# Kernel optimization log

Measured on AMD Instinct MI355X. Metric: run time of the kernel, lower is better.

Reference implementation:

```python
import jax, jax.numpy as jnp
import numpy as np

N_NODES = 100000


def sage_conv(x, edge_index, Wl, bl, Wr):
    # PyG SAGEConv (aggr='mean', root_weight=True):
    #   out_i = lin_l(mean_{j in N(i)} x_j) + lin_r(x_i)
    src, dst = edge_index[0], edge_index[1]
    msgs = x[src]  # [E, C] gather of source-node features
    summed = jax.ops.segment_sum(msgs, dst, num_segments=N_NODES)
    deg = jax.ops.segment_sum(jnp.ones((edge_index.shape[1],), x.dtype), dst,
                              num_segments=N_NODES)
    mean = summed / jnp.maximum(deg, 1.0)[:, None]  # zero rows stay zero
    return mean @ Wl.T + bl + x @ Wr.T


def setup_inputs() -> dict:
    key = jax.random.key(0)
    ks = jax.random.split(key, 12)
    IN, HID, OUT = 128, 128, 64
    E, P = 1600000, 200000
    x = jax.random.normal(ks[0], (N_NODES, IN), jnp.float32)
    edge_index = jax.random.randint(ks[1], (2, E), 0, N_NODES)
    edge_label_index = jax.random.randint(ks[2], (2, P), 0, N_NODES)
    s1 = 1.0 / np.sqrt(IN)
    s2 = 1.0 / np.sqrt(HID)
    s3 = 1.0 / np.sqrt(2 * OUT)
    return {
        "x": x,
        "edge_index": edge_index,
        "edge_label_index": edge_label_index,
        "Wl1": jax.random.uniform(ks[3], (HID, IN), jnp.float32, -s1, s1),
        "bl1": jnp.zeros((HID,), jnp.float32),
        "Wr1": jax.random.uniform(ks[4], (HID, IN), jnp.float32, -s1, s1),
        "Wl2": jax.random.uniform(ks[5], (OUT, HID), jnp.float32, -s2, s2),
        "bl2": jnp.zeros((OUT,), jnp.float32),
        "Wr2": jax.random.uniform(ks[6], (OUT, HID), jnp.float32, -s2, s2),
        "Wdec": jax.random.uniform(ks[7], (1, 2 * OUT), jnp.float32, -s3, s3),
        "bdec": jax.random.uniform(ks[8], (1,), jnp.float32, -s3, s3),
    }


def reference(x, edge_index, edge_label_index, Wl1, bl1, Wr1, Wl2, bl2, Wr2,
              Wdec, bdec):
    # encode: SAGEConv -> relu -> (dropout p=0) -> SAGEConv
    h = jax.nn.relu(sage_conv(x, edge_index, Wl1, bl1, Wr1))
    z = sage_conv(h, edge_index, Wl2, bl2, Wr2)
    # decode: gather endpoint embeddings, concat, linear -> [P]
    feats = jnp.concatenate([z[edge_label_index[0]], z[edge_label_index[1]]],
                            axis=-1)
    return (feats @ Wdec.T + bdec).reshape(-1)
```

## Files before the change

kernel.cpp:

```cpp
#include <hip/hip_runtime.h>

#define NN 100000
#define NBUK ((NN + 255) / 256)
#define BCAP 5120

typedef unsigned short u16;
typedef unsigned int u32;
typedef __attribute__((ext_vector_type(8))) short short8v;
typedef __attribute__((ext_vector_type(4))) float float4v;

__device__ __forceinline__ u32 f2bf_rne(float f) {
    u32 x = __float_as_uint(f);
    return (x + 0x7fffu + ((x >> 16) & 1u)) >> 16;
}
__device__ __forceinline__ float bf2f(u32 u) {
    return __uint_as_float(u << 16);
}
__device__ __forceinline__ uint4 pack8u(const float4& a, const float4& b) {
    uint4 u;
    u.x = f2bf_rne(a.x) | (f2bf_rne(a.y) << 16);
    u.y = f2bf_rne(a.z) | (f2bf_rne(a.w) << 16);
    u.z = f2bf_rne(b.x) | (f2bf_rne(b.y) << 16);
    u.w = f2bf_rne(b.z) | (f2bf_rne(b.w) << 16);
    return u;
}

__global__ void zero_buckets_kernel(int* __restrict__ p) {
    int i = threadIdx.x;
    if (i < NBUK) p[i] = 0;
}

__global__ __launch_bounds__(256) void partition_kernel(const int* __restrict__ edges,
                                                        int* __restrict__ bucketCnt,
                                                        int* __restrict__ bucketed, int E) {
    __shared__ int h[NBUK];
    __shared__ int base[NBUK];
    for (int i = threadIdx.x; i < NBUK; i += 256) h[i] = 0;
    __syncthreads();
    int b0 = blockIdx.x * 4096;
    for (int k = threadIdx.x; k < 4096; k += 256) {
        int e = b0 + k;
        if (e < E) atomicAdd(&h[edges[E + e] >> 8], 1);
    }
    __syncthreads();
    for (int i = threadIdx.x; i < NBUK; i += 256) {
        int c = h[i];
        base[i] = c ? (i * BCAP + atomicAdd(&bucketCnt[i], c)) : 0;
        h[i] = 0;
    }
    __syncthreads();
    for (int k = threadIdx.x; k < 4096; k += 256) {
        int e = b0 + k;
        if (e < E) {
            int d = edges[E + e];
            int b = d >> 8;
            int off = atomicAdd(&h[b], 1);
            bucketed[base[b] + off] = edges[e] | ((d & 255) << 20);
        }
    }
}

__global__ __launch_bounds__(256) void bucket_sort_kernel(const int* __restrict__ bucketed,
                                                          const int* __restrict__ bucketCnt,
                                                          int* __restrict__ rowStart,
                                                          int* __restrict__ cnt,
                                                          int* __restrict__ sortedSrc, int N) {
    __shared__ int h[256];
    __shared__ int pos[256];
    int b = blockIdx.x;
    int tid = threadIdx.x;
    int start = b * BCAP, end = start + bucketCnt[b];
    h[tid] = 0;
    __syncthreads();
    for (int k = start + tid; k < end; k += 256) atomicAdd(&h[bucketed[k] >> 20], 1);
    __syncthreads();
    int v = h[tid];
    pos[tid] = v;
    __syncthreads();
    for (int off = 1; off < 256; off <<= 1) {
        int t = (tid >= off) ? pos[tid - off] : 0;
        __syncthreads();
        pos[tid] += t;
        __syncthreads();
    }
    int excl = start + pos[tid] - v;
    int node = (b << 8) + tid;
    if (node < N) {
        rowStart[node] = excl;
        cnt[node] = v;
    }
    h[tid] = excl;
    __syncthreads();
    for (int k = start + tid; k < end; k += 256) {
        int entry = bucketed[k];
        int p = atomicAdd(&h[entry >> 20], 1);
        sortedSrc[p] = entry & 0xFFFFF;
    }
}

template <bool XF32>
__global__ __launch_bounds__(256, 2) void gemm_mfma_kernel(
    const void* __restrict__ Xv, const float* __restrict__ Wa,
    const float* __restrict__ Wb, int CHALF,
    u16* __restrict__ Ob, int OSTRIDE, int N)
{
    __shared__ u16 As[128 * 128];

    const int tid = threadIdx.x;
    const int w = tid >> 6;
    const int l = tid & 63;
    const int l15 = l & 15;
    const int lhi = l >> 4;
    const int rowBase = blockIdx.x * 128;
    const int cBase = blockIdx.y * 128;
    char* asb = reinterpret_cast<char*>(As);

#pragma unroll
    for (int i = 0; i < 8; ++i) {
        int q = tid + i * 256;
        int r = q >> 4, c = q & 15;
        int gr = rowBase + r;
        uint4 pk = make_uint4(0u, 0u, 0u, 0u);
        if (gr < N) {
            if (XF32) {
                const float* xf = (const float*)Xv + (size_t)gr * 128 + c * 8;
                float4 f0 = *reinterpret_cast<const float4*>(xf);
                float4 f1 = *reinterpret_cast<const float4*>(xf + 4);
                pk = pack8u(f0, f1);
            } else {
                pk = *reinterpret_cast<const uint4*>((const u16*)Xv + (size_t)gr * 128 + c * 8);
            }
        }
        *reinterpret_cast<uint4*>(asb + r * 256 + ((c * 16) ^ ((r & 7) << 4))) = pk;
    }

    short8v bfrag[2][4];
#pragma unroll
    for (int nj = 0; nj < 2; ++nj) {
        int c = cBase + w * 32 + nj * 16 + l15;
        const float* wr = (c < CHALF) ? (Wa + (size_t)c * 128)
                                      : (Wb + (size_t)(c - CHALF) * 128);
#pragma unroll
        for (int kk = 0; kk < 4; ++kk) {
            float4 f0 = *reinterpret_cast<const float4*>(wr + kk * 32 + lhi * 8);
            float4 f1 = *reinterpret_cast<const float4*>(wr + kk * 32 + lhi * 8 + 4);
            uint4 pk = pack8u(f0, f1);
            union { uint4 u; short8v s; } cv; cv.u = pk;
            bfrag[nj][kk] = cv.s;
        }
    }

    __syncthreads();

    float4v acc[8][2];
    const float4v az = {0.f, 0.f, 0.f, 0.f};
#pragma unroll
    for (int mi = 0; mi < 8; ++mi) { acc[mi][0] = az; acc[mi][1] = az; }

#pragma unroll
    for (int kk = 0; kk < 4; ++kk) {
#pragma unroll
        for (int mi = 0; mi < 8; ++mi) {
            int r = mi * 16 + l15;
            short8v a = *reinterpret_cast<const short8v*>(
                asb + r * 256 + ((kk * 64 + lhi * 16) ^ ((r & 7) << 4)));
            acc[mi][0] = __builtin_amdgcn_mfma_f32_16x16x32_bf16(a, bfrag[0][kk], acc[mi][0], 0, 0, 0);
            acc[mi][1] = __builtin_amdgcn_mfma_f32_16x16x32_bf16(a, bfrag[1][kk], acc[mi][1], 0, 0, 0);
        }
    }

#pragma unroll
    for (int mi = 0; mi < 8; ++mi) {
#pragma unroll
        for (int nj = 0; nj < 2; ++nj) {
            int gc = cBase + w * 32 + nj * 16 + l15;
#pragma unroll
            for (int j = 0; j < 4; ++j) {
                int gr = rowBase + mi * 16 + lhi * 4 + j;
                if (gr < N) Ob[(size_t)gr * OSTRIDE + gc] = (u16)f2bf_rne(acc[mi][nj][j]);
            }
        }
    }
}

template <bool RELU>
__global__ __launch_bounds__(256) void agg_combine_kernel(
    const u16* __restrict__ T, int tStride,
    const u16* __restrict__ R,
    const int* __restrict__ sortedSrc, const int* __restrict__ rowStart,
    const int* __restrict__ cnt, const float* __restrict__ bias,
    u16* __restrict__ outB, int oStride, int N)
{
    constexpr int TPN = 8;
    constexpr int NPB = 256 / TPN;
    int n = blockIdx.x * NPB + threadIdx.x / TPN;
    int c = threadIdx.x % TPN;
    if (n >= N) return;
    int start = rowStart[n];
    int m = cnt[n];
    const int* __restrict__ ep = sortedSrc + start;
    const u16* __restrict__ tp = T + c * 8;

    float a0 = 0.f, a1 = 0.f, a2 = 0.f, a3 = 0.f;
    float a4 = 0.f, a5 = 0.f, a6 = 0.f, a7 = 0.f;
    int k = 0;
    for (; k + 8 <= m; k += 8) {
        int s[8];
        uint4 v[8];
#pragma unroll
        for (int u = 0; u < 8; ++u) s[u] = ep[k + u];
#pragma unroll
        for (int u = 0; u < 8; ++u)
            v[u] = *reinterpret_cast<const uint4*>(&tp[(size_t)s[u] * tStride]);
#pragma unroll
        for (int h = 0; h < 2; ++h) {
            const uint4& w0 = v[h * 4 + 0]; const uint4& w1 = v[h * 4 + 1];
            const uint4& w2 = v[h * 4 + 2]; const uint4& w3 = v[h * 4 + 3];
            a0 += bf2f(w0.x & 0xffffu) + bf2f(w1.x & 0xffffu) + bf2f(w2.x & 0xffffu) + bf2f(w3.x & 0xffffu);
            a1 += bf2f(w0.x >> 16) + bf2f(w1.x >> 16) + bf2f(w2.x >> 16) + bf2f(w3.x >> 16);
            a2 += bf2f(w0.y & 0xffffu) + bf2f(w1.y & 0xffffu) + bf2f(w2.y & 0xffffu) + bf2f(w3.y & 0xffffu);
            a3 += bf2f(w0.y >> 16) + bf2f(w1.y >> 16) + bf2f(w2.y >> 16) + bf2f(w3.y >> 16);
            a4 += bf2f(w0.z & 0xffffu) + bf2f(w1.z & 0xffffu) + bf2f(w2.z & 0xffffu) + bf2f(w3.z & 0xffffu);
            a5 += bf2f(w0.z >> 16) + bf2f(w1.z >> 16) + bf2f(w2.z >> 16) + bf2f(w3.z >> 16);
            a6 += bf2f(w0.w & 0xffffu) + bf2f(w1.w & 0xffffu) + bf2f(w2.w & 0xffffu) + bf2f(w3.w & 0xffffu);
            a7 += bf2f(w0.w >> 16) + bf2f(w1.w >> 16) + bf2f(w2.w >> 16) + bf2f(w3.w >> 16);
        }
    }
    for (; k + 4 <= m; k += 4) {
        int s0 = ep[k], s1 = ep[k + 1], s2 = ep[k + 2], s3 = ep[k + 3];
        uint4 w0 = *reinterpret_cast<const uint4*>(&tp[(size_t)s0 * tStride]);
        uint4 w1 = *reinterpret_cast<const uint4*>(&tp[(size_t)s1 * tStride]);
        uint4 w2 = *reinterpret_cast<const uint4*>(&tp[(size_t)s2 * tStride]);
        uint4 w3 = *reinterpret_cast<const uint4*>(&tp[(size_t)s3 * tStride]);
        a0 += bf2f(w0.x & 0xffffu) + bf2f(w1.x & 0xffffu) + bf2f(w2.x & 0xffffu) + bf2f(w3.x & 0xffffu);
        a1 += bf2f(w0.x >> 16) + bf2f(w1.x >> 16) + bf2f(w2.x >> 16) + bf2f(w3.x >> 16);
        a2 += bf2f(w0.y & 0xffffu) + bf2f(w1.y & 0xffffu) + bf2f(w2.y & 0xffffu) + bf2f(w3.y & 0xffffu);
        a3 += bf2f(w0.y >> 16) + bf2f(w1.y >> 16) + bf2f(w2.y >> 16) + bf2f(w3.y >> 16);
        a4 += bf2f(w0.z & 0xffffu) + bf2f(w1.z & 0xffffu) + bf2f(w2.z & 0xffffu) + bf2f(w3.z & 0xffffu);
        a5 += bf2f(w0.z >> 16) + bf2f(w1.z >> 16) + bf2f(w2.z >> 16) + bf2f(w3.z >> 16);
        a6 += bf2f(w0.w & 0xffffu) + bf2f(w1.w & 0xffffu) + bf2f(w2.w & 0xffffu) + bf2f(w3.w & 0xffffu);
        a7 += bf2f(w0.w >> 16) + bf2f(w1.w >> 16) + bf2f(w2.w >> 16) + bf2f(w3.w >> 16);
    }
    for (; k < m; ++k) {
        uint4 v = *reinterpret_cast<const uint4*>(&tp[(size_t)ep[k] * tStride]);
        a0 += bf2f(v.x & 0xffffu); a1 += bf2f(v.x >> 16);
        a2 += bf2f(v.y & 0xffffu); a3 += bf2f(v.y >> 16);
        a4 += bf2f(v.z & 0xffffu); a5 += bf2f(v.z >> 16);
        a6 += bf2f(v.w & 0xffffu); a7 += bf2f(v.w >> 16);
    }
    float inv = 1.0f / fmaxf((float)m, 1.0f);
    uint4 rv = *reinterpret_cast<const uint4*>(&R[(size_t)n * tStride + c * 8]);
    float o0 = fmaf(a0, inv, bias[c * 8 + 0]) + bf2f(rv.x & 0xffffu);
    float o1 = fmaf(a1, inv, bias[c * 8 + 1]) + bf2f(rv.x >> 16);
    float o2 = fmaf(a2, inv, bias[c * 8 + 2]) + bf2f(rv.y & 0xffffu);
    float o3 = fmaf(a3, inv, bias[c * 8 + 3]) + bf2f(rv.y >> 16);
    float o4 = fmaf(a4, inv, bias[c * 8 + 4]) + bf2f(rv.z & 0xffffu);
    float o5 = fmaf(a5, inv, bias[c * 8 + 5]) + bf2f(rv.z >> 16);
    float o6 = fmaf(a6, inv, bias[c * 8 + 6]) + bf2f(rv.w & 0xffffu);
    float o7 = fmaf(a7, inv, bias[c * 8 + 7]) + bf2f(rv.w >> 16);
    if (RELU) {
        o0 = fmaxf(o0, 0.f); o1 = fmaxf(o1, 0.f);
        o2 = fmaxf(o2, 0.f); o3 = fmaxf(o3, 0.f);
        o4 = fmaxf(o4, 0.f); o5 = fmaxf(o5, 0.f);
        o6 = fmaxf(o6, 0.f); o7 = fmaxf(o7, 0.f);
    }
    uint4 o;
    o.x = f2bf_rne(o0) | (f2bf_rne(o1) << 16);
    o.y = f2bf_rne(o2) | (f2bf_rne(o3) << 16);
    o.z = f2bf_rne(o4) | (f2bf_rne(o5) << 16);
    o.w = f2bf_rne(o6) | (f2bf_rne(o7) << 16);
    *reinterpret_cast<uint4*>(&outB[(size_t)n * oStride + c * 8]) = o;
}

__global__ __launch_bounds__(256) void decode_kernel(
    const u16* __restrict__ z, const int* __restrict__ eli,
    const float* __restrict__ Wdec, const float* __restrict__ bdec,
    float* __restrict__ out, int P)
{
    int t = blockIdx.x * 256 + threadIdx.x;
    int p = t >> 6;
    int lane = t & 63;
    if (p >= P) return;
    int a = eli[p];
    int b = eli[P + p];
    float acc = bf2f(z[(size_t)a * 64 + lane]) * Wdec[lane]
              + bf2f(z[(size_t)b * 64 + lane]) * Wdec[64 + lane];
    for (int off = 32; off; off >>= 1) acc += __shfl_down(acc, off);
    if (lane == 0) out[p] = acc + bdec[0];
}

extern "C" void kernel_launch(void* const* d_in, const int* in_sizes, int n_in,
                              void* d_out, int out_size, void* d_ws, size_t ws_size,
                              hipStream_t stream) {
    const float* x    = (const float*)d_in[0];
    const int*   ei   = (const int*)d_in[1];
    const int*   eli  = (const int*)d_in[2];
    const float* Wl1  = (const float*)d_in[3];
    const float* bl1  = (const float*)d_in[4];
    const float* Wr1  = (const float*)d_in[5];
    const float* Wl2  = (const float*)d_in[6];
    const float* bl2  = (const float*)d_in[7];
    const float* Wr2  = (const float*)d_in[8];
    const float* Wdec = (const float*)d_in[9];
    const float* bdec = (const float*)d_in[10];
    float* out = (float*)d_out;

    const int N = NN;
    const int E = in_sizes[1] / 2;
    const int P = in_sizes[2] / 2;
    const int EB = (E + 4095) / 4096;

    char* wp = (char*)d_ws;
    u16* obf = (u16*)wp;  wp += (size_t)N * 256 * 2;
    u16* hbf = (u16*)wp;  wp += (size_t)N * 128 * 2;
    u16* zb  = (u16*)wp;  wp += (size_t)N * 64 * 2;
    int* bucketCnt = (int*)wp;
    int* rowStart  = bucketCnt + NBUK;
    int* cnt       = rowStart + N;
    int* bucketed  = cnt + N;
    int* sortedSrc = bucketed + NBUK * BCAP;

    zero_buckets_kernel<<<1, 512, 0, stream>>>(bucketCnt);
    partition_kernel<<<EB, 256, 0, stream>>>(ei, bucketCnt, bucketed, E);
    bucket_sort_kernel<<<NBUK, 256, 0, stream>>>(bucketed, bucketCnt, rowStart, cnt, sortedSrc, N);

    {
        dim3 grid((N + 127) / 128, 2);
        gemm_mfma_kernel<true><<<grid, 256, 0, stream>>>(x, Wl1, Wr1, 128, obf, 256, N);
    }
    agg_combine_kernel<true><<<(N + 31) / 32, 256, 0, stream>>>(
        obf, 256, obf + 128, sortedSrc, rowStart, cnt, bl1, hbf, 128, N);
    agg_combine_kernel<true><<<(N + 31) / 32, 256, 0, stream>>>(
        obf + 64, 256, obf + 192, sortedSrc, rowStart, cnt, bl1 + 64, hbf + 64, 128, N);

    {
        dim3 grid((N + 127) / 128, 1);
        gemm_mfma_kernel<false><<<grid, 256, 0, stream>>>(hbf, Wl2, Wr2, 64, obf, 128, N);
    }
    agg_combine_kernel<false><<<(N + 31) / 32, 256, 0, stream>>>(
        obf, 128, obf + 64, sortedSrc, rowStart, cnt, bl2, zb, 64, N);

    decode_kernel<<<(P + 3) / 4, 256, 0, stream>>>(zb, eli, Wdec, bdec, out, P);
}
```

Before: 241.9 us.

## Stage GEMM output through LDS for coalesced stores; merge layer-1 aggregation halves

The GEMM epilogue now writes bf16 results into swizzled shared memory and then stores each row as 16-byte vectors to global memory, replacing scattered 2-byte stores. The layer-1 aggregation, which ran as two 64-column launches, becomes a single 128-column launch with 16 threads per node. The merge means each node's edge list and indices are read once instead of twice, at the cost of twice as many threads per node. The extra syncthreads and LDS round trip add a little latency to the GEMM.

```diff
diff --git a/kernel.cpp b/kernel.cpp
--- a/kernel.cpp
+++ b/kernel.cpp
@@ -169,29 +169,43 @@
         }
     }
 
+    __syncthreads();
 #pragma unroll
     for (int mi = 0; mi < 8; ++mi) {
 #pragma unroll
         for (int nj = 0; nj < 2; ++nj) {
-            int gc = cBase + w * 32 + nj * 16 + l15;
+            int cc = w * 32 + nj * 16 + l15;
 #pragma unroll
             for (int j = 0; j < 4; ++j) {
-                int gr = rowBase + mi * 16 + lhi * 4 + j;
-                if (gr < N) Ob[(size_t)gr * OSTRIDE + gc] = (u16)f2bf_rne(acc[mi][nj][j]);
+                int r = mi * 16 + lhi * 4 + j;
+                *reinterpret_cast<u16*>(asb + r * 256 + ((cc * 2) ^ ((r & 7) << 4)))
+                    = (u16)f2bf_rne(acc[mi][nj][j]);
             }
         }
     }
-}
-
-template <bool RELU>
+    __syncthreads();
+#pragma unroll
+    for (int i = 0; i < 8; ++i) {
+        int q = tid + i * 256;
+        int r = q >> 4, c = q & 15;
+        int gr = rowBase + r;
+        if (gr < N) {
+            uint4 v = *reinterpret_cast<const uint4*>(
+                asb + r * 256 + ((c * 16) ^ ((r & 7) << 4)));
+            *reinterpret_cast<uint4*>(&Ob[(size_t)gr * OSTRIDE + cBase + c * 8]) = v;
+        }
+    }
+}
+
+template <int C, bool RELU>
 __global__ __launch_bounds__(256) void agg_combine_kernel(
     const u16* __restrict__ T, int tStride,
     const u16* __restrict__ R,
     const int* __restrict__ sortedSrc, const int* __restrict__ rowStart,
     const int* __restrict__ cnt, const float* __restrict__ bias,
-    u16* __restrict__ outB, int oStride, int N)
+    u16* __restrict__ outB, int N)
 {
-    constexpr int TPN = 8;
+    constexpr int TPN = C / 8;
     constexpr int NPB = 256 / TPN;
     int n = blockIdx.x * NPB + threadIdx.x / TPN;
     int c = threadIdx.x % TPN;
@@ -269,7 +283,7 @@
     o.y = f2bf_rne(o2) | (f2bf_rne(o3) << 16);
     o.z = f2bf_rne(o4) | (f2bf_rne(o5) << 16);
     o.w = f2bf_rne(o6) | (f2bf_rne(o7) << 16);
-    *reinterpret_cast<uint4*>(&outB[(size_t)n * oStride + c * 8]) = o;
+    *reinterpret_cast<uint4*>(&outB[(size_t)n * C + c * 8]) = o;
 }
 
 __global__ __launch_bounds__(256) void decode_kernel(
@@ -328,17 +342,15 @@
         dim3 grid((N + 127) / 128, 2);
         gemm_mfma_kernel<true><<<grid, 256, 0, stream>>>(x, Wl1, Wr1, 128, obf, 256, N);
     }
-    agg_combine_kernel<true><<<(N + 31) / 32, 256, 0, stream>>>(
-        obf, 256, obf + 128, sortedSrc, rowStart, cnt, bl1, hbf, 128, N);
-    agg_combine_kernel<true><<<(N + 31) / 32, 256, 0, stream>>>(
-        obf + 64, 256, obf + 192, sortedSrc, rowStart, cnt, bl1 + 64, hbf + 64, 128, N);
+    agg_combine_kernel<128, true><<<(N + 15) / 16, 256, 0, stream>>>(
+        obf, 256, obf + 128, sortedSrc, rowStart, cnt, bl1, hbf, N);
 
     {
         dim3 grid((N + 127) / 128, 1);
         gemm_mfma_kernel<false><<<grid, 256, 0, stream>>>(hbf, Wl2, Wr2, 64, obf, 128, N);
     }
-    agg_combine_kernel<false><<<(N + 31) / 32, 256, 0, stream>>>(
-        obf, 128, obf + 64, sortedSrc, rowStart, cnt, bl2, zb, 64, N);
+    agg_combine_kernel<64, false><<<(N + 31) / 32, 256, 0, stream>>>(
+        obf, 128, obf + 64, sortedSrc, rowStart, cnt, bl2, zb, N);
 
     decode_kernel<<<(P + 3) / 4, 256, 0, stream>>>(zb, eli, Wdec, bdec, out, P);
 }
```

Result: faster. 233.4 us (-3.5%).
